# Performance work log

Measured on AMD Instinct MI355X. Metric: run time of the kernel, lower is better.

Reference implementation:

```python
import jax, jax.numpy as jnp
import numpy as np

N, E, D_IN, D_OUT = 50000, 1600000, 256, 256


def setup_inputs() -> dict:
    key = jax.random.key(0)
    k1, k2, k3, k4, k5, k6 = jax.random.split(key, 6)
    x = jax.random.normal(k1, (N, D_IN), dtype=jnp.float32)
    edge_index = jax.random.randint(k2, (2, E), 0, N, dtype=jnp.int64)
    s = 1.0 / np.sqrt(D_IN)
    W1 = jax.random.uniform(k3, (D_OUT, D_IN), minval=-s, maxval=s, dtype=jnp.float32)
    b1 = jax.random.uniform(k4, (D_OUT,), minval=-s, maxval=s, dtype=jnp.float32)
    W2 = jax.random.uniform(k5, (D_OUT, D_IN), minval=-s, maxval=s, dtype=jnp.float32)
    b2 = jax.random.uniform(k6, (D_OUT,), minval=-s, maxval=s, dtype=jnp.float32)
    return {"x": x, "W1": W1, "b1": b1, "W2": W2, "b2": b2, "edge_index": edge_index}


def reference(x, W1, b1, W2, b2, edge_index):
    # edge_index[0] = destination node, edge_index[1] = neighbor (as in the torch loop)
    dst = edge_index[0]
    nbr = edge_index[1]
    n = x.shape[0]
    # segment mean of neighbor features per destination node
    agg = jax.ops.segment_sum(x[nbr], dst, num_segments=n)  # [N, D_IN]
    cnt = jax.ops.segment_sum(jnp.ones((nbr.shape[0],), x.dtype), dst, num_segments=n)
    mean = agg / jnp.maximum(cnt, 1.0)[:, None]  # isolated nodes -> 0 (torch gives NaN)
    return x @ W1.T + b1 + mean @ W2.T + b2
```

## Files before the change

kernel.cpp:

```cpp
#include <hip/hip_runtime.h>
#include <hip/hip_bf16.h>
#include <hip/hip_fp8.h>

typedef __bf16 bf16x4 __attribute__((ext_vector_type(4)));
typedef __bf16 bf16x8 __attribute__((ext_vector_type(8)));
typedef float f32x4 __attribute__((ext_vector_type(4)));
typedef float f32x2 __attribute__((ext_vector_type(2)));

#define D_IN 256
#define D_OUT 256
#define K_DIM 512
#define PAD 96
#define NBIN 640
#define NPS 79
#define BINCAP2 12
#define ROUND1 3072
#define CVT_BLK 1024
#define CONVW_BLK 512


__device__ __forceinline__ unsigned int pack4_fp8(float a, float b, float c, float d) {
#if __has_builtin(__builtin_amdgcn_cvt_pk_fp8_f32)
    int r = 0;
    r = __builtin_amdgcn_cvt_pk_fp8_f32(a, b, r, false);
    r = __builtin_amdgcn_cvt_pk_fp8_f32(c, d, r, true);
    return (unsigned int)r;
#else
    union { unsigned int u; unsigned char by[4]; } v;
    v.by[0] = __hip_fp8_e4m3(a).__x;
    v.by[1] = __hip_fp8_e4m3(b).__x;
    v.by[2] = __hip_fp8_e4m3(c).__x;
    v.by[3] = __hip_fp8_e4m3(d).__x;
    return v.u;
#endif
}

__device__ __forceinline__ void unpack4_fp8(unsigned int u, f32x2& lo, f32x2& hi) {
#if __has_builtin(__builtin_amdgcn_cvt_pk_f32_fp8)
    lo = __builtin_amdgcn_cvt_pk_f32_fp8(u, false);
    hi = __builtin_amdgcn_cvt_pk_f32_fp8(u, true);
#else
    union { unsigned int uu; unsigned char by[4]; } v; v.uu = u;
    __hip_fp8_e4m3 q0, q1, q2, q3;
    q0.__x = v.by[0]; q1.__x = v.by[1]; q2.__x = v.by[2]; q3.__x = v.by[3];
    lo[0] = (float)q0; lo[1] = (float)q1; hi[0] = (float)q2; hi[1] = (float)q3;
#endif
}


__global__ __launch_bounds__(256) void prep_kernel(const int* __restrict__ dst,
                                                   const int* __restrict__ nbr,
                                                   unsigned int* __restrict__ bins,
                                                   int* __restrict__ bin_cnt,
                                                   const float* __restrict__ x,
                                                   unsigned int* __restrict__ x8,
                                                   __bf16* __restrict__ xb,
                                                   const float* __restrict__ W1,
                                                   const float* __restrict__ W2,
                                                   const float* __restrict__ b1,
                                                   const float* __restrict__ b2,
                                                   __bf16* __restrict__ Wbuf,
                                                   float* __restrict__ bias,
                                                   int E, int n8, int subCap, int nSub) {
    __shared__ unsigned int buf[NBIN][BINCAP2];
    __shared__ int bcnt[NBIN];
    __shared__ int bbase[NBIN];
    const int tid = threadIdx.x;
    const int bid = blockIdx.x;

    if (bid < nSub) {
        for (int b = tid; b < NBIN; b += 256) bcnt[b] = 0;
        __syncthreads();
        const int base = bid * ROUND1;
        const int hi = min(E, base + ROUND1);
        for (int e = base + tid; e < hi; e += 256) {
            int d  = __builtin_nontemporal_load(dst + e);
            int nb = __builtin_nontemporal_load(nbr + e);
            int s = d / NPS;
            unsigned int packed = ((unsigned int)d << 16) | (unsigned int)nb;
            int pos = atomicAdd(&bcnt[s], 1);
            if (pos < BINCAP2) {
                buf[s][pos] = packed;
            } else {
                int gp = atomicAdd(&bin_cnt[s], 1);
                if (gp < subCap) bins[(size_t)s * subCap + gp] = packed;
            }
        }
        __syncthreads();
        for (int b = tid; b < NBIN; b += 256) {
            int c = min(bcnt[b], BINCAP2);
            bbase[b] = atomicAdd(&bin_cnt[b], c);
        }
        __syncthreads();
        const int wave = tid >> 6, lane = tid & 63;
        for (int b = wave; b < NBIN; b += 4) {
            int c = min(bcnt[b], BINCAP2);
            if (lane < c)
                __builtin_nontemporal_store(buf[b][lane], &bins[(size_t)b * subCap + bbase[b] + lane]);
        }
    } else if (bid < nSub + CVT_BLK) {
        int i = (bid - nSub) * 256 + tid;
        for (; i < n8; i += CVT_BLK * 256) {
            const float4* p = (const float4*)(x + (size_t)i * 8);
            float4 a = p[0], b = p[1];
            uint2 o;
            o.x = pack4_fp8(a.x, a.y, a.z, a.w);
            o.y = pack4_fp8(b.x, b.y, b.z, b.w);
            *(uint2*)(x8 + (size_t)i * 2) = o;
            bf16x8 hb = { (__bf16)a.x, (__bf16)a.y, (__bf16)a.z, (__bf16)a.w,
                          (__bf16)b.x, (__bf16)b.y, (__bf16)b.z, (__bf16)b.w };
            *(bf16x8*)(xb + (size_t)i * 8) = hb;
        }
    } else {
        int i = (bid - nSub - CVT_BLK) * 256 + tid;
        int o = i >> 9;
        int k = i & 511;
        float v = (k < D_IN) ? W1[o * D_IN + k] : W2[o * D_IN + (k - D_IN)];
        Wbuf[i] = (__bf16)v;
        if (i < D_OUT) bias[i] = b1[i] + b2[i];
    }
}


__global__ __launch_bounds__(256) void fillgather_kernel(const unsigned int* __restrict__ x8,
                                                         const unsigned int* __restrict__ bins,
                                                         const int* __restrict__ bin_cnt,
                                                         __bf16* __restrict__ Mbuf,
                                                         int subCap, int N) {
    __shared__ unsigned short lbuck[NPS][PAD];
    __shared__ int lcnt[NPS];
    const int s = blockIdx.x;
    const int node0 = s * NPS;
    const int tid = threadIdx.x;

    for (int i = tid; i < NPS; i += 256) lcnt[i] = 0;
    __syncthreads();

    const int cnt = min(bin_cnt[s], subCap);
    const size_t sbase = (size_t)s * subCap;
    for (int i = tid; i < cnt; i += 256) {
        unsigned int p = bins[sbase + i];
        int nl = (int)(p >> 16) - node0;
        int pos = atomicAdd(&lcnt[nl], 1);
        if (pos < PAD) lbuck[nl][pos] = (unsigned short)(p & 0xffffu);
    }
    __syncthreads();

    const int wave = tid >> 6, lane = tid & 63;
    for (int nl = wave; nl < NPS; nl += 4) {
        int node = node0 + nl;
        if (node >= N) continue;
        int c = min(lcnt[nl], PAD);
        const unsigned int* bw = (const unsigned int*)(&lbuck[nl][0]);

        f32x2 a0lo = {0.f,0.f}, a0hi = {0.f,0.f};
        f32x2 a1lo = {0.f,0.f}, a1hi = {0.f,0.f};
        f32x2 a2lo = {0.f,0.f}, a2hi = {0.f,0.f};
        f32x2 a3lo = {0.f,0.f}, a3hi = {0.f,0.f};

        int i = 0;
        for (; i + 16 <= c; i += 16) {
            int ib = i >> 1;
            unsigned int w0 = bw[ib+0], w1 = bw[ib+1], w2 = bw[ib+2], w3 = bw[ib+3];
            unsigned int w4 = bw[ib+4], w5 = bw[ib+5], w6 = bw[ib+6], w7 = bw[ib+7];
            unsigned int u0  = x8[(size_t)(w0 & 0xffffu) * 64 + lane];
            unsigned int u1  = x8[(size_t)(w0 >> 16)     * 64 + lane];
            unsigned int u2  = x8[(size_t)(w1 & 0xffffu) * 64 + lane];
            unsigned int u3  = x8[(size_t)(w1 >> 16)     * 64 + lane];
            unsigned int u4  = x8[(size_t)(w2 & 0xffffu) * 64 + lane];
            unsigned int u5  = x8[(size_t)(w2 >> 16)     * 64 + lane];
            unsigned int u6  = x8[(size_t)(w3 & 0xffffu) * 64 + lane];
            unsigned int u7  = x8[(size_t)(w3 >> 16)     * 64 + lane];
            unsigned int u8  = x8[(size_t)(w4 & 0xffffu) * 64 + lane];
            unsigned int u9  = x8[(size_t)(w4 >> 16)     * 64 + lane];
            unsigned int u10 = x8[(size_t)(w5 & 0xffffu) * 64 + lane];
            unsigned int u11 = x8[(size_t)(w5 >> 16)     * 64 + lane];
            unsigned int u12 = x8[(size_t)(w6 & 0xffffu) * 64 + lane];
            unsigned int u13 = x8[(size_t)(w6 >> 16)     * 64 + lane];
            unsigned int u14 = x8[(size_t)(w7 & 0xffffu) * 64 + lane];
            unsigned int u15 = x8[(size_t)(w7 >> 16)     * 64 + lane];
            f32x2 lo, hi;
            unpack4_fp8(u0,  lo, hi); a0lo += lo; a0hi += hi;
            unpack4_fp8(u1,  lo, hi); a1lo += lo; a1hi += hi;
            unpack4_fp8(u2,  lo, hi); a2lo += lo; a2hi += hi;
            unpack4_fp8(u3,  lo, hi); a3lo += lo; a3hi += hi;
            unpack4_fp8(u4,  lo, hi); a0lo += lo; a0hi += hi;
            unpack4_fp8(u5,  lo, hi); a1lo += lo; a1hi += hi;
            unpack4_fp8(u6,  lo, hi); a2lo += lo; a2hi += hi;
            unpack4_fp8(u7,  lo, hi); a3lo += lo; a3hi += hi;
            unpack4_fp8(u8,  lo, hi); a0lo += lo; a0hi += hi;
            unpack4_fp8(u9,  lo, hi); a1lo += lo; a1hi += hi;
            unpack4_fp8(u10, lo, hi); a2lo += lo; a2hi += hi;
            unpack4_fp8(u11, lo, hi); a3lo += lo; a3hi += hi;
            unpack4_fp8(u12, lo, hi); a0lo += lo; a0hi += hi;
            unpack4_fp8(u13, lo, hi); a1lo += lo; a1hi += hi;
            unpack4_fp8(u14, lo, hi); a2lo += lo; a2hi += hi;
            unpack4_fp8(u15, lo, hi); a3lo += lo; a3hi += hi;
        }
        for (; i + 4 <= c; i += 4) {
            int ib = i >> 1;
            unsigned int w0 = bw[ib+0], w1 = bw[ib+1];
            unsigned int u0 = x8[(size_t)(w0 & 0xffffu) * 64 + lane];
            unsigned int u1 = x8[(size_t)(w0 >> 16)     * 64 + lane];
            unsigned int u2 = x8[(size_t)(w1 & 0xffffu) * 64 + lane];
            unsigned int u3 = x8[(size_t)(w1 >> 16)     * 64 + lane];
            f32x2 lo, hi;
            unpack4_fp8(u0, lo, hi); a0lo += lo; a0hi += hi;
            unpack4_fp8(u1, lo, hi); a1lo += lo; a1hi += hi;
            unpack4_fp8(u2, lo, hi); a2lo += lo; a2hi += hi;
            unpack4_fp8(u3, lo, hi); a3lo += lo; a3hi += hi;
        }
        for (; i < c; i++) {
            unsigned int u0 = x8[(size_t)lbuck[nl][i] * 64 + lane];
            f32x2 lo, hi;
            unpack4_fp8(u0, lo, hi); a0lo += lo; a0hi += hi;
        }
        a0lo += a1lo + a2lo + a3lo;
        a0hi += a1hi + a2hi + a3hi;
        float inv = (c > 0) ? 1.0f / (float)c : 0.0f;
        bf16x4 hm = { (__bf16)(a0lo[0] * inv), (__bf16)(a0lo[1] * inv),
                      (__bf16)(a0hi[0] * inv), (__bf16)(a0hi[1] * inv) };
        *(bf16x4*)(Mbuf + (size_t)node * D_IN + lane * 4) = hm;
    }
}


__global__ __launch_bounds__(512, 5) void gemm_kernel(const __bf16* __restrict__ xb,
                                                      const __bf16* __restrict__ Mb,
                                                      const __bf16* __restrict__ W,
                                                      const float* __restrict__ bias,
                                                      float* __restrict__ out, int M) {
    __shared__ __bf16 As[64][40];
    __shared__ __bf16 Ws[256][40];

    const int tid = threadIdx.x;
    const int lane = tid & 63;
    const int wave = tid >> 6;
    const int wr = wave >> 2;
    const int wc = wave & 3;
    const int brow = blockIdx.x * 64;

    f32x4 acc[2][4];
    #pragma unroll
    for (int m = 0; m < 2; m++)
        #pragma unroll
        for (int n = 0; n < 4; n++)
            acc[m][n] = (f32x4){0.f, 0.f, 0.f, 0.f};

    const int lr = lane & 15;
    const int lg8 = (lane >> 4) * 8;

    const int rowA = tid >> 2;
    const int chA  = (tid & 3) * 8;
    const int growA = brow + rowA;
    const bool aOK = (tid < 256) && (growA < M);
    const int rowW0 = tid >> 2;
    const int rowW1 = (512 + tid) >> 2;
    const int chW = (tid & 3) * 8;

    bf16x8 rA = {};
    bf16x8 rW0, rW1;

    if (aOK) rA = *(const bf16x8*)(xb + (size_t)growA * D_IN + chA);
    rW0 = *(const bf16x8*)(W + (size_t)rowW0 * K_DIM + chW);
    rW1 = *(const bf16x8*)(W + (size_t)rowW1 * K_DIM + chW);

    for (int kk = 0; kk < 16; kk++) {
        if (tid < 256) *(bf16x8*)(&As[rowA][chA]) = rA;
        *(bf16x8*)(&Ws[rowW0][chW]) = rW0;
        *(bf16x8*)(&Ws[rowW1][chW]) = rW1;
        __syncthreads();

        if (kk < 15) {
            const int kn = (kk + 1) * 32;
            const __bf16* srcA = (kn < D_IN) ? xb : Mb;
            if (aOK) rA = *(const bf16x8*)(srcA + (size_t)growA * D_IN + (kn & (D_IN - 1)) + chA);
            rW0 = *(const bf16x8*)(W + (size_t)rowW0 * K_DIM + kn + chW);
            rW1 = *(const bf16x8*)(W + (size_t)rowW1 * K_DIM + kn + chW);
        }

        bf16x8 af[2], wf[4];
        #pragma unroll
        for (int m = 0; m < 2; m++) af[m] = *(const bf16x8*)(&As[wr * 32 + m * 16 + lr][lg8]);
        #pragma unroll
        for (int n = 0; n < 4; n++) wf[n] = *(const bf16x8*)(&Ws[wc * 64 + n * 16 + lr][lg8]);

        #pragma unroll
        for (int m = 0; m < 2; m++)
            #pragma unroll
            for (int n = 0; n < 4; n++)
                acc[m][n] = __builtin_amdgcn_mfma_f32_16x16x32_bf16(af[m], wf[n], acc[m][n], 0, 0, 0);
        __syncthreads();
    }

    const int lg = lane >> 4;
    #pragma unroll
    for (int nf = 0; nf < 4; nf++) {
        int col = wc * 64 + nf * 16 + lr;
        float bv = bias[col];
        #pragma unroll
        for (int mf = 0; mf < 2; mf++) {
            int row0 = brow + wr * 32 + mf * 16 + lg * 4;
            #pragma unroll
            for (int j = 0; j < 4; j++) {
                int row = row0 + j;
                if (row < M) out[(size_t)row * D_OUT + col] = acc[mf][nf][j] + bv;
            }
        }
    }
}


extern "C" void kernel_launch(void* const* d_in, const int* in_sizes, int n_in,
                              void* d_out, int out_size, void* d_ws, size_t ws_size,
                              hipStream_t stream) {
    const float* x  = (const float*)d_in[0];
    const float* W1 = (const float*)d_in[1];
    const float* b1 = (const float*)d_in[2];
    const float* W2 = (const float*)d_in[3];
    const float* b2 = (const float*)d_in[4];
    const int* edges = (const int*)d_in[5];

    const int N = in_sizes[0] / D_IN;
    const int E = in_sizes[5] / 2;
    const int* dst = edges;
    const int* nbr = edges + E;
    const int subCap = (E / NBIN) * 3 / 2 + 64;

    char* ws = (char*)d_ws;
    size_t woff = 0;
    auto alloc = [&](size_t bytes) -> void* {
        void* p = ws + woff;
        woff = (woff + bytes + 255) & ~(size_t)255;
        return p;
    };
    unsigned int* x8 = (unsigned int*)alloc((size_t)N * D_IN);
    __bf16* xb   = (__bf16*)alloc((size_t)N * D_IN * 2);
    __bf16* Mbuf = (__bf16*)alloc((size_t)N * D_IN * 2);
    __bf16* Wbuf = (__bf16*)alloc((size_t)D_OUT * K_DIM * 2);
    float*  bias = (float*)alloc(D_OUT * 4);
    int* bin_cnt = (int*)alloc(NBIN * 4);
    unsigned int* bins = (unsigned int*)alloc((size_t)NBIN * subCap * 4);

    const int nSub = (E + ROUND1 - 1) / ROUND1;
    const int n8 = N * D_IN / 8;

    hipMemsetAsync(bin_cnt, 0, NBIN * 4, stream);
    prep_kernel<<<nSub + CVT_BLK + CONVW_BLK, 256, 0, stream>>>(
        dst, nbr, bins, bin_cnt, x, x8, xb, W1, W2, b1, b2, Wbuf, bias, E, n8, subCap, nSub);

    int fgBlocks = (N + NPS - 1) / NPS;
    fillgather_kernel<<<fgBlocks, 256, 0, stream>>>(x8, bins, bin_cnt, Mbuf, subCap, N);

    int nblk = (N + 63) / 64;
    gemm_kernel<<<nblk, 512, 0, stream>>>(xb, Mbuf, Wbuf, bias, (float*)d_out, N);
}
```

Baseline: 159.0 us.

## Replace atomic edge binning with histogram, scan and deterministic placement passes

```diff
diff --git a/kernel.cpp b/kernel.cpp
--- a/kernel.cpp
+++ b/kernel.cpp
@@ -13,8 +13,8 @@
 #define PAD 96
 #define NBIN 640
 #define NPS 79
-#define BINCAP2 12
 #define ROUND1 3072
+#define CAP3 20
 #define CVT_BLK 1024
 #define CONVW_BLK 512
 
@@ -49,9 +49,7 @@
 
 
 __global__ __launch_bounds__(256) void prep_kernel(const int* __restrict__ dst,
-                                                   const int* __restrict__ nbr,
-                                                   unsigned int* __restrict__ bins,
-                                                   int* __restrict__ bin_cnt,
+                                                   unsigned int* __restrict__ hist,
                                                    const float* __restrict__ x,
                                                    unsigned int* __restrict__ x8,
                                                    __bf16* __restrict__ xb,
@@ -61,43 +59,23 @@
                                                    const float* __restrict__ b2,
                                                    __bf16* __restrict__ Wbuf,
                                                    float* __restrict__ bias,
-                                                   int E, int n8, int subCap, int nSub) {
-    __shared__ unsigned int buf[NBIN][BINCAP2];
+                                                   int E, int n8, int nSub) {
     __shared__ int bcnt[NBIN];
-    __shared__ int bbase[NBIN];
     const int tid = threadIdx.x;
     const int bid = blockIdx.x;
 
     if (bid < nSub) {
-        for (int b = tid; b < NBIN; b += 256) bcnt[b] = 0;
+        for (int s = tid; s < NBIN; s += 256) bcnt[s] = 0;
         __syncthreads();
         const int base = bid * ROUND1;
         const int hi = min(E, base + ROUND1);
         for (int e = base + tid; e < hi; e += 256) {
-            int d  = __builtin_nontemporal_load(dst + e);
-            int nb = __builtin_nontemporal_load(nbr + e);
-            int s = d / NPS;
-            unsigned int packed = ((unsigned int)d << 16) | (unsigned int)nb;
-            int pos = atomicAdd(&bcnt[s], 1);
-            if (pos < BINCAP2) {
-                buf[s][pos] = packed;
-            } else {
-                int gp = atomicAdd(&bin_cnt[s], 1);
-                if (gp < subCap) bins[(size_t)s * subCap + gp] = packed;
-            }
+            int d = __builtin_nontemporal_load(dst + e);
+            atomicAdd(&bcnt[d / NPS], 1);
         }
         __syncthreads();
-        for (int b = tid; b < NBIN; b += 256) {
-            int c = min(bcnt[b], BINCAP2);
-            bbase[b] = atomicAdd(&bin_cnt[b], c);
-        }
-        __syncthreads();
-        const int wave = tid >> 6, lane = tid & 63;
-        for (int b = wave; b < NBIN; b += 4) {
-            int c = min(bcnt[b], BINCAP2);
-            if (lane < c)
-                __builtin_nontemporal_store(buf[b][lane], &bins[(size_t)b * subCap + bbase[b] + lane]);
-        }
+        for (int s = tid; s < NBIN; s += 256)
+            hist[(size_t)bid * NBIN + s] = (unsigned int)bcnt[s];
     } else if (bid < nSub + CVT_BLK) {
         int i = (bid - nSub) * 256 + tid;
         for (; i < n8; i += CVT_BLK * 256) {
@@ -122,24 +100,84 @@
 }
 
 
-__global__ __launch_bounds__(256) void fillgather_kernel(const unsigned int* __restrict__ x8,
+__global__ __launch_bounds__(64) void scan_kernel(const unsigned int* __restrict__ hist,
+                                                  unsigned int* __restrict__ sbase,
+                                                  int* __restrict__ bin_cnt, int nSub) {
+    const int s = blockIdx.x;
+    const int lane = threadIdx.x;
+    unsigned int carry = 0;
+    for (int b0 = 0; b0 < nSub; b0 += 64) {
+        int b = b0 + lane;
+        unsigned int v = (b < nSub) ? hist[(size_t)b * NBIN + s] : 0u;
+        unsigned int sc = v;
+        #pragma unroll
+        for (int d = 1; d < 64; d <<= 1) {
+            unsigned int t = __shfl_up(sc, d, 64);
+            if (lane >= d) sc += t;
+        }
+        if (b < nSub) sbase[(size_t)b * NBIN + s] = carry + sc - v;
+        carry += __shfl(sc, 63, 64);
+    }
+    if (lane == 0) bin_cnt[s] = (int)carry;
+}
+
+
+__global__ __launch_bounds__(256) void place_kernel(const int* __restrict__ dst,
+                                                    const int* __restrict__ nbr,
+                                                    const unsigned int* __restrict__ sbase,
+                                                    unsigned int* __restrict__ bins,
+                                                    int E, int segCap, int nSub) {
+    __shared__ unsigned int buf[NBIN][CAP3];
+    __shared__ int bcnt[NBIN];
+    __shared__ unsigned int gbase[NBIN];
+    const int tid = threadIdx.x;
+    const int bid = blockIdx.x;
+
+    for (int s = tid; s < NBIN; s += 256) {
+        bcnt[s] = 0;
+        gbase[s] = sbase[(size_t)bid * NBIN + s];
+    }
+    __syncthreads();
+
+    const int base = bid * ROUND1;
+    const int hi = min(E, base + ROUND1);
+    for (int e = base + tid; e < hi; e += 256) {
+        int d  = __builtin_nontemporal_load(dst + e);
+        int nb = __builtin_nontemporal_load(nbr + e);
+        int s = d / NPS;
+        unsigned int packed = ((unsigned int)d << 16) | (unsigned int)nb;
+        int pos = atomicAdd(&bcnt[s], 1);
+        if (pos < CAP3) buf[s][pos] = packed;
+        else bins[(size_t)s * segCap + gbase[s] + pos] = packed;
+    }
+    __syncthreads();
+
+    const int wave = tid >> 6, lane = tid & 63;
+    for (int s = wave; s < NBIN; s += 4) {
+        int c = min(bcnt[s], CAP3);
+        if (lane < c) bins[(size_t)s * segCap + gbase[s] + lane] = buf[s][lane];
+    }
+}
+
+
+__global__ __launch_bounds__(512) void fillgather_kernel(const unsigned int* __restrict__ x8,
                                                          const unsigned int* __restrict__ bins,
                                                          const int* __restrict__ bin_cnt,
                                                          __bf16* __restrict__ Mbuf,
-                                                         int subCap, int N) {
+                                                         int segCap, int N) {
     __shared__ unsigned short lbuck[NPS][PAD];
     __shared__ int lcnt[NPS];
     const int s = blockIdx.x;
     const int node0 = s * NPS;
     const int tid = threadIdx.x;
 
-    for (int i = tid; i < NPS; i += 256) lcnt[i] = 0;
+    for (int i = tid; i < NPS; i += 512) lcnt[i] = 0;
     __syncthreads();
 
-    const int cnt = min(bin_cnt[s], subCap);
-    const size_t sbase = (size_t)s * subCap;
-    for (int i = tid; i < cnt; i += 256) {
-        unsigned int p = bins[sbase + i];
+    const int cnt = min(bin_cnt[s], segCap);
+    const size_t sbase_ = (size_t)s * segCap;
+    for (int i = tid; i < cnt; i += 512) {
+        unsigned int p = bins[sbase_ + i];
         int nl = (int)(p >> 16) - node0;
         int pos = atomicAdd(&lcnt[nl], 1);
         if (pos < PAD) lbuck[nl][pos] = (unsigned short)(p & 0xffffu);
@@ -147,7 +185,7 @@
     __syncthreads();
 
     const int wave = tid >> 6, lane = tid & 63;
-    for (int nl = wave; nl < NPS; nl += 4) {
+    for (int nl = wave; nl < NPS; nl += 8) {
         int node = node0 + nl;
         if (node >= N) continue;
         int c = min(lcnt[nl], PAD);
@@ -325,7 +363,9 @@
     const int E = in_sizes[5] / 2;
     const int* dst = edges;
     const int* nbr = edges + E;
-    const int subCap = (E / NBIN) * 3 / 2 + 64;
+    const int segCap = (E / NBIN) * 3 / 2 + 64;
+    const int nSub = (E + ROUND1 - 1) / ROUND1;
+    const int n8 = N * D_IN / 8;
 
     char* ws = (char*)d_ws;
     size_t woff = 0;
@@ -340,17 +380,17 @@
     __bf16* Wbuf = (__bf16*)alloc((size_t)D_OUT * K_DIM * 2);
     float*  bias = (float*)alloc(D_OUT * 4);
     int* bin_cnt = (int*)alloc(NBIN * 4);
-    unsigned int* bins = (unsigned int*)alloc((size_t)NBIN * subCap * 4);
-
-    const int nSub = (E + ROUND1 - 1) / ROUND1;
-    const int n8 = N * D_IN / 8;
-
-    hipMemsetAsync(bin_cnt, 0, NBIN * 4, stream);
+    unsigned int* hist  = (unsigned int*)alloc((size_t)nSub * NBIN * 4);
+    unsigned int* sbase = (unsigned int*)alloc((size_t)nSub * NBIN * 4);
+    unsigned int* bins  = (unsigned int*)alloc((size_t)NBIN * segCap * 4);
+
     prep_kernel<<<nSub + CVT_BLK + CONVW_BLK, 256, 0, stream>>>(
-        dst, nbr, bins, bin_cnt, x, x8, xb, W1, W2, b1, b2, Wbuf, bias, E, n8, subCap, nSub);
+        dst, hist, x, x8, xb, W1, W2, b1, b2, Wbuf, bias, E, n8, nSub);
+    scan_kernel<<<NBIN, 64, 0, stream>>>(hist, sbase, bin_cnt, nSub);
+    place_kernel<<<nSub, 256, 0, stream>>>(dst, nbr, sbase, bins, E, segCap, nSub);
 
     int fgBlocks = (N + NPS - 1) / NPS;
-    fillgather_kernel<<<fgBlocks, 256, 0, stream>>>(x8, bins, bin_cnt, Mbuf, subCap, N);
+    fillgather_kernel<<<fgBlocks, 512, 0, stream>>>(x8, bins, bin_cnt, Mbuf, segCap, N);
 
     int nblk = (N + 63) / 64;
     gemm_kernel<<<nblk, 512, 0, stream>>>(xb, Mbuf, Wbuf, bias, (float*)d_out, N);
```

Result: slower. 170.7 us (+7.4%).
